# Performance work log

Hardware: AMD Instinct MI355X
Metric: run time of the kernel (lower is better)

The kernel has to match this reference:

```python
import jax, jax.numpy as jnp
import numpy as np
import itertools

BINS_NUM = 35
BINS_SIZE = 9
ORDERS = (2, 3, 4, 5)

def _comb_idx(n, k):
    # combinations with replacement of indices 0..n-1, shape [ncomb, k]
    return np.array(list(itertools.combinations_with_replacement(range(n), k)), dtype=np.int32)

_COMB = {k: _comb_idx(BINS_SIZE, k) for k in ORDERS}


def setup_inputs() -> dict:
    key = jax.random.key(0)
    x = jax.random.normal(key, (1024, BINS_NUM * BINS_SIZE), dtype=jnp.float32)
    return {"x": x}


def reference(x) -> jnp.ndarray:
    B = x.shape[0]
    bins = x.reshape(B, BINS_NUM, BINS_SIZE)          # [B, 35, 9]
    parts = [bins]                                     # 'origin' slice first
    for k in ORDERS:
        idx = jnp.asarray(_COMB[k])                    # [ncomb_k, k]
        gathered = bins[:, :, idx]                     # [B, 35, ncomb_k, k]
        parts.append(jnp.prod(gathered, axis=-1))      # [B, 35, ncomb_k]
    # per-bin concat [origin, de2, de3, de4, de5], then flatten bins -> matches
    # torch's outer concat over bins since bin is the leading concat axis here.
    out = jnp.concatenate(parts, axis=-1)              # [B, 35, 2001]
    return out.reshape(B, -1)                          # [B, 70035]
```

## Files before the change

### kernel.cpp

```cpp
#include <hip/hip_runtime.h>

#define NBIN 35
#define BSZ 9
#define NOUT_PER_BIN 2001

struct PackTab { unsigned pk[NOUT_PER_BIN]; };

constexpr PackTab make_tab() {
    PackTab t{};
    int p = 0;
    constexpr unsigned S = 9;
    for (unsigned a = 0; a < 9; ++a)
        t.pk[p++] = a | (S << 4) | (S << 8) | (S << 12) | (S << 16);
    for (unsigned a = 0; a < 9; ++a)
        for (unsigned b = a; b < 9; ++b)
            t.pk[p++] = a | (b << 4) | (S << 8) | (S << 12) | (S << 16);
    for (unsigned a = 0; a < 9; ++a)
        for (unsigned b = a; b < 9; ++b)
            for (unsigned c = b; c < 9; ++c)
                t.pk[p++] = a | (b << 4) | (c << 8) | (S << 12) | (S << 16);
    for (unsigned a = 0; a < 9; ++a)
        for (unsigned b = a; b < 9; ++b)
            for (unsigned c = b; c < 9; ++c)
                for (unsigned d = c; d < 9; ++d)
                    t.pk[p++] = a | (b << 4) | (c << 8) | (d << 12) | (S << 16);
    for (unsigned a = 0; a < 9; ++a)
        for (unsigned b = a; b < 9; ++b)
            for (unsigned c = b; c < 9; ++c)
                for (unsigned d = c; d < 9; ++d)
                    for (unsigned e = d; e < 9; ++e)
                        t.pk[p++] = a | (b << 4) | (c << 8) | (d << 12) | (e << 16);
    return t;
}

__constant__ PackTab g_tab = make_tab();

__global__ __launch_bounds__(256) void poly_expand_kernel(
        const float* __restrict__ x, float* __restrict__ out, int ntask) {
    __shared__ float vs[4][12];
    const int wave = threadIdx.x >> 6;
    const int lane = threadIdx.x & 63;
    const int task = blockIdx.x * 4 + wave;
    const bool valid = task < ntask;

    if (valid && lane < 10) {
        vs[wave][lane] = (lane < 9) ? x[(size_t)task * BSZ + lane] : 1.0f;
    }
    __syncthreads();
    if (!valid) return;

    const float* v = vs[wave];
    const size_t base = (size_t)task * NOUT_PER_BIN;

    for (int j0 = 0; j0 < NOUT_PER_BIN; j0 += 64) {
        const int j = j0 + lane;
        if (j < NOUT_PER_BIN) {
            const unsigned pk = g_tab.pk[j];
            float p = v[pk & 15u];
            p *= v[(pk >> 4) & 15u];
            p *= v[(pk >> 8) & 15u];
            p *= v[(pk >> 12) & 15u];
            p *= v[(pk >> 16) & 15u];
            out[base + j] = p;
        }
    }
}

extern "C" void kernel_launch(void* const* d_in, const int* in_sizes, int n_in,
                              void* d_out, int out_size, void* d_ws, size_t ws_size,
                              hipStream_t stream) {
    const float* x = (const float*)d_in[0];
    float* out = (float*)d_out;
    const int B = in_sizes[0] / (NBIN * BSZ);
    const int ntask = B * NBIN;
    const int blocks = (ntask + 3) / 4;
    poly_expand_kernel<<<blocks, 256, 0, stream>>>(x, out, ntask);
}
```

Baseline: 60.61 us.

## Split output into flat aligned chunks with float4 stores and precomputed pair products

Work is now split over the flat output in 1024-element chunks instead of one 2001-element bin per wave. Each chunk spans at most two bins, and a magic-number division maps each element to its bin. Each lane computes four consecutive outputs and writes them with one float4 store, so stores are wide and aligned instead of scalar stores at odd per-bin offsets. Pairwise products are precomputed in LDS so each output takes three lookups instead of five. The cost is per-element division arithmetic and the per-wave setup for the second bin.

```diff
diff --git a/kernel.cpp b/kernel.cpp
--- a/kernel.cpp
+++ b/kernel.cpp
@@ -1,67 +1,112 @@
 #include <hip/hip_runtime.h>
 
-#define NBIN 35
 #define BSZ 9
-#define NOUT_PER_BIN 2001
+#define NPB 2001
+#define CHUNK 1024
+#define REG 56
+#define MAGIC 137370269ULL
+#define MSHIFT 38
 
-struct PackTab { unsigned pk[NOUT_PER_BIN]; };
+constexpr unsigned pslot(unsigned i, unsigned j) {
+    return 9u + i * 9u - i * (i - 1u) / 2u + (j - i);
+}
 
-constexpr PackTab make_tab() {
-    PackTab t{};
+struct Tab3 { unsigned pk[NPB]; };
+constexpr Tab3 make_tab3() {
+    Tab3 t{};
     int p = 0;
-    constexpr unsigned S = 9;
+    constexpr unsigned ONE = 54;
     for (unsigned a = 0; a < 9; ++a)
-        t.pk[p++] = a | (S << 4) | (S << 8) | (S << 12) | (S << 16);
+        t.pk[p++] = a | (ONE << 6) | (ONE << 12);
     for (unsigned a = 0; a < 9; ++a)
         for (unsigned b = a; b < 9; ++b)
-            t.pk[p++] = a | (b << 4) | (S << 8) | (S << 12) | (S << 16);
+            t.pk[p++] = pslot(a, b) | (ONE << 6) | (ONE << 12);
     for (unsigned a = 0; a < 9; ++a)
         for (unsigned b = a; b < 9; ++b)
             for (unsigned c = b; c < 9; ++c)
-                t.pk[p++] = a | (b << 4) | (c << 8) | (S << 12) | (S << 16);
+                t.pk[p++] = pslot(a, b) | (c << 6) | (ONE << 12);
     for (unsigned a = 0; a < 9; ++a)
         for (unsigned b = a; b < 9; ++b)
             for (unsigned c = b; c < 9; ++c)
                 for (unsigned d = c; d < 9; ++d)
-                    t.pk[p++] = a | (b << 4) | (c << 8) | (d << 12) | (S << 16);
+                    t.pk[p++] = pslot(a, b) | (pslot(c, d) << 6) | (ONE << 12);
     for (unsigned a = 0; a < 9; ++a)
         for (unsigned b = a; b < 9; ++b)
             for (unsigned c = b; c < 9; ++c)
                 for (unsigned d = c; d < 9; ++d)
                     for (unsigned e = d; e < 9; ++e)
-                        t.pk[p++] = a | (b << 4) | (c << 8) | (d << 12) | (e << 16);
+                        t.pk[p++] = pslot(a, b) | (pslot(c, d) << 6) | (e << 12);
     return t;
 }
+__constant__ Tab3 g_tab = make_tab3();
 
-__constant__ PackTab g_tab = make_tab();
+struct PTab { unsigned ij[45]; };
+constexpr PTab make_ptab() {
+    PTab t{};
+    int p = 0;
+    for (unsigned i = 0; i < 9; ++i)
+        for (unsigned j = i; j < 9; ++j)
+            t.ij[p++] = i | (j << 8);
+    return t;
+}
+__constant__ PTab g_ptab = make_ptab();
 
 __global__ __launch_bounds__(256) void poly_expand_kernel(
-        const float* __restrict__ x, float* __restrict__ out, int ntask) {
-    __shared__ float vs[4][12];
+        const float* __restrict__ x, float* __restrict__ out,
+        unsigned out_n, unsigned ntask) {
+    __shared__ float L[4][2][REG];
     const int wave = threadIdx.x >> 6;
     const int lane = threadIdx.x & 63;
-    const int task = blockIdx.x * 4 + wave;
-    const bool valid = task < ntask;
+    const unsigned chunk = blockIdx.x * 4u + wave;
+    const unsigned g0 = chunk * CHUNK;
+    if (g0 >= out_n) return;
 
-    if (valid && lane < 10) {
-        vs[wave][lane] = (lane < 9) ? x[(size_t)task * BSZ + lane] : 1.0f;
+    const unsigned t0 = (unsigned)(((unsigned long long)g0 * MAGIC) >> MSHIFT);
+    unsigned gLastEl = g0 + CHUNK - 1;
+    if (gLastEl >= out_n) gLastEl = out_n - 1;
+    const unsigned tLast = (unsigned)(((unsigned long long)gLastEl * MAGIC) >> MSHIFT);
+    const bool twoTasks = (tLast > t0);
+    const unsigned t1 = twoTasks ? (t0 + 1u) : t0;
+
+    float (*Lw)[REG] = L[wave];
+
+    if (lane < 9)                         Lw[0][lane]      = x[t0 * BSZ + lane];
+    else if (lane == 9)                   Lw[0][54]        = 1.0f;
+    else if (lane >= 16 && lane < 25)     Lw[1][lane - 16] = x[t1 * BSZ + (lane - 16)];
+    else if (lane == 25)                  Lw[1][54]        = 1.0f;
+    __builtin_amdgcn_wave_barrier();
+
+    if (lane < 45) {
+        const unsigned ij = g_ptab.ij[lane];
+        Lw[0][9 + lane] = Lw[0][ij & 255u] * Lw[0][ij >> 8];
     }
-    __syncthreads();
-    if (!valid) return;
+    if (twoTasks && lane < 45) {
+        const unsigned ij = g_ptab.ij[lane];
+        Lw[1][9 + lane] = Lw[1][ij & 255u] * Lw[1][ij >> 8];
+    }
+    __builtin_amdgcn_wave_barrier();
 
-    const float* v = vs[wave];
-    const size_t base = (size_t)task * NOUT_PER_BIN;
-
-    for (int j0 = 0; j0 < NOUT_PER_BIN; j0 += 64) {
-        const int j = j0 + lane;
-        if (j < NOUT_PER_BIN) {
+    const float* Lb = &Lw[0][0];
+    #pragma unroll
+    for (int it = 0; it < 4; ++it) {
+        const unsigned gb = g0 + (unsigned)(it * 256 + lane * 4);
+        if (gb >= out_n) continue;
+        float r[4];
+        #pragma unroll
+        for (int e = 0; e < 4; ++e) {
+            const unsigned g = gb + (unsigned)e;
+            const unsigned t = (unsigned)(((unsigned long long)g * MAGIC) >> MSHIFT);
+            const unsigned j = g - t * (unsigned)NPB;
+            const float* Ls = Lb + (t - t0) * REG;
             const unsigned pk = g_tab.pk[j];
-            float p = v[pk & 15u];
-            p *= v[(pk >> 4) & 15u];
-            p *= v[(pk >> 8) & 15u];
-            p *= v[(pk >> 12) & 15u];
-            p *= v[(pk >> 16) & 15u];
-            out[base + j] = p;
+            r[e] = Ls[pk & 63u] * Ls[(pk >> 6) & 63u] * Ls[(pk >> 12) & 63u];
+        }
+        if (gb + 4u <= out_n) {
+            *reinterpret_cast<float4*>(out + gb) =
+                make_float4(r[0], r[1], r[2], r[3]);
+        } else {
+            for (unsigned e = 0; e < 4 && gb + e < out_n; ++e)
+                out[gb + e] = r[e];
         }
     }
 }
@@ -71,8 +116,9 @@
                               hipStream_t stream) {
     const float* x = (const float*)d_in[0];
     float* out = (float*)d_out;
-    const int B = in_sizes[0] / (NBIN * BSZ);
-    const int ntask = B * NBIN;
-    const int blocks = (ntask + 3) / 4;
-    poly_expand_kernel<<<blocks, 256, 0, stream>>>(x, out, ntask);
+    const unsigned ntask = (unsigned)(in_sizes[0] / BSZ);
+    const unsigned out_n = (unsigned)out_size;
+    const unsigned nchunk = (out_n + CHUNK - 1) / CHUNK;
+    const unsigned blocks = (nchunk + 3) / 4;
+    poly_expand_kernel<<<blocks, 256, 0, stream>>>(x, out, out_n, ntask);
 }
```

New measurement: 82.82 us. +36.7%, slower.

## Build monomials incrementally from lower-order products staged in shared memory

Applied to the files above, without the earlier changes.

Each order-k monomial is now formed as one multiply of a cached order-(k-1) product and a single input value, instead of five table-driven multiplies per output. Orders up to four are built level by level in a per-wave shared-memory buffer, with block-wide barriers between levels, and the order-5 terms are written straight to global memory. The goal is to cut ALU work and constant-table traffic per output. In exchange it adds about 11 KB of LDS per block and several synchronisations, and floating-point products may round slightly differently. The kernel already writes close to its full output size, so store bandwidth likely dominates the runtime.

```diff
diff --git a/kernel.cpp b/kernel.cpp
--- a/kernel.cpp
+++ b/kernel.cpp
@@ -1,67 +1,118 @@
 #include <hip/hip_runtime.h>
 
-#define NBIN 35
 #define BSZ 9
-#define NOUT_PER_BIN 2001
+#define NPB 2001
+#define N2 45
+#define N3 165
+#define N4 495
+#define N5 1287
+#define O2 9
+#define O3 54
+#define O4 219
+#define O5 714
+#define LSLOTS 720
 
-struct PackTab { unsigned pk[NOUT_PER_BIN]; };
+constexpr unsigned pslot2(unsigned i, unsigned j) {
+    return O2 + i * 9u - i * (i - 1u) / 2u + (j - i);
+}
 
-constexpr PackTab make_tab() {
-    PackTab t{};
-    int p = 0;
-    constexpr unsigned S = 9;
-    for (unsigned a = 0; a < 9; ++a)
-        t.pk[p++] = a | (S << 4) | (S << 8) | (S << 12) | (S << 16);
-    for (unsigned a = 0; a < 9; ++a)
-        for (unsigned b = a; b < 9; ++b)
-            t.pk[p++] = a | (b << 4) | (S << 8) | (S << 12) | (S << 16);
-    for (unsigned a = 0; a < 9; ++a)
-        for (unsigned b = a; b < 9; ++b)
-            for (unsigned c = b; c < 9; ++c)
-                t.pk[p++] = a | (b << 4) | (c << 8) | (S << 12) | (S << 16);
-    for (unsigned a = 0; a < 9; ++a)
-        for (unsigned b = a; b < 9; ++b)
-            for (unsigned c = b; c < 9; ++c)
-                for (unsigned d = c; d < 9; ++d)
-                    t.pk[p++] = a | (b << 4) | (c << 8) | (d << 12) | (S << 16);
-    for (unsigned a = 0; a < 9; ++a)
-        for (unsigned b = a; b < 9; ++b)
-            for (unsigned c = b; c < 9; ++c)
-                for (unsigned d = c; d < 9; ++d)
-                    for (unsigned e = d; e < 9; ++e)
-                        t.pk[p++] = a | (b << 4) | (c << 8) | (d << 12) | (e << 16);
+struct Tabs {
+    unsigned short p2[N2];
+    unsigned short p3[N3];
+    unsigned short p4[N4];
+    unsigned short p5[N5];
+};
+constexpr Tabs make_tabs() {
+    Tabs t{};
+    { int p = 0;
+      for (unsigned i = 0; i < 9; ++i)
+          for (unsigned j = i; j < 9; ++j)
+              t.p2[p++] = (unsigned short)(i | (j << 8)); }
+    { int p = 0;
+      for (unsigned a = 0; a < 9; ++a)
+          for (unsigned b = a; b < 9; ++b) {
+              const unsigned ps = pslot2(a, b);
+              for (unsigned c = b; c < 9; ++c)
+                  t.p3[p++] = (unsigned short)(ps | (c << 8));
+          } }
+    { int p = 0; unsigned ts = O3;
+      for (unsigned a = 0; a < 9; ++a)
+          for (unsigned b = a; b < 9; ++b)
+              for (unsigned c = b; c < 9; ++c) {
+                  for (unsigned d = c; d < 9; ++d)
+                      t.p4[p++] = (unsigned short)(ts | (d << 8));
+                  ++ts;
+              } }
+    { int p = 0; unsigned qs = O4;
+      for (unsigned a = 0; a < 9; ++a)
+          for (unsigned b = a; b < 9; ++b)
+              for (unsigned c = b; c < 9; ++c)
+                  for (unsigned d = c; d < 9; ++d) {
+                      for (unsigned e = d; e < 9; ++e)
+                          t.p5[p++] = (unsigned short)(qs | (e << 10));
+                      ++qs;
+                  } }
     return t;
 }
-
-__constant__ PackTab g_tab = make_tab();
+__constant__ Tabs g_tabs = make_tabs();
 
 __global__ __launch_bounds__(256) void poly_expand_kernel(
         const float* __restrict__ x, float* __restrict__ out, int ntask) {
-    __shared__ float vs[4][12];
+    __shared__ float L[4][LSLOTS];
     const int wave = threadIdx.x >> 6;
     const int lane = threadIdx.x & 63;
     const int task = blockIdx.x * 4 + wave;
     const bool valid = task < ntask;
+    float* Lw = L[wave];
 
-    if (valid && lane < 10) {
-        vs[wave][lane] = (lane < 9) ? x[(size_t)task * BSZ + lane] : 1.0f;
+    if (valid && lane < 9) Lw[lane] = x[(size_t)task * BSZ + lane];
+    __syncthreads();
+
+    if (valid && lane < N2) {
+        const unsigned pk = g_tabs.p2[lane];
+        Lw[O2 + lane] = Lw[pk & 255u] * Lw[pk >> 8];
     }
     __syncthreads();
+
+    if (valid) {
+        #pragma unroll
+        for (int k = 0; k < 3; ++k) {
+            const int s = lane + 64 * k;
+            if (s < N3) {
+                const unsigned pk = g_tabs.p3[s];
+                Lw[O3 + s] = Lw[pk & 255u] * Lw[pk >> 8];
+            }
+        }
+    }
+    __syncthreads();
+
+    if (valid) {
+        #pragma unroll
+        for (int k = 0; k < 8; ++k) {
+            const int s = lane + 64 * k;
+            if (s < N4) {
+                const unsigned pk = g_tabs.p4[s];
+                Lw[O4 + s] = Lw[pk & 255u] * Lw[pk >> 8];
+            }
+        }
+    }
+    __syncthreads();
+
     if (!valid) return;
+    const unsigned base = (unsigned)task * NPB;
 
-    const float* v = vs[wave];
-    const size_t base = (size_t)task * NOUT_PER_BIN;
+    #pragma unroll
+    for (int k = 0; k < 12; ++k) {
+        const int j = lane + 64 * k;
+        if (j < O5) out[base + j] = Lw[j];
+    }
 
-    for (int j0 = 0; j0 < NOUT_PER_BIN; j0 += 64) {
-        const int j = j0 + lane;
-        if (j < NOUT_PER_BIN) {
-            const unsigned pk = g_tab.pk[j];
-            float p = v[pk & 15u];
-            p *= v[(pk >> 4) & 15u];
-            p *= v[(pk >> 8) & 15u];
-            p *= v[(pk >> 12) & 15u];
-            p *= v[(pk >> 16) & 15u];
-            out[base + j] = p;
+    #pragma unroll 4
+    for (int k = 0; k < 21; ++k) {
+        const int s = lane + 64 * k;
+        if (s < N5) {
+            const unsigned pk = g_tabs.p5[s];
+            out[base + O5 + s] = Lw[pk & 1023u] * Lw[pk >> 10];
         }
     }
 }
@@ -71,8 +122,7 @@
                               hipStream_t stream) {
     const float* x = (const float*)d_in[0];
     float* out = (float*)d_out;
-    const int B = in_sizes[0] / (NBIN * BSZ);
-    const int ntask = B * NBIN;
+    const int ntask = in_sizes[0] / BSZ;
     const int blocks = (ntask + 3) / 4;
     poly_expand_kernel<<<blocks, 256, 0, stream>>>(x, out, ntask);
 }
```

Result: slower. 64.97 us (+7.2%).
